# Optimization experiments

Hardware: AMD Instinct MI355X
Metric: run time of the kernel (lower is better)

## Reference

```python
import jax, jax.numpy as jnp
import numpy as np
import math

B, D, NSTEPS = 16384, 256, 5
TEMP, ALPHA, ALPHA_A, ETA, EPS = 2.0, 0.2, 0.5, 1.0e4, 1e-10


def setup_inputs() -> dict:
    key = jax.random.key(0)
    ks = jax.random.split(key, 7)
    x = jax.random.bernoulli(ks[0], 0.5, (B, D)).astype(jnp.float32)  # binary state
    x_a = jax.random.normal(ks[1], (B, D), jnp.float32)  # auxiliary (continuous)
    A = jax.random.normal(ks[2], (D, D), jnp.float32)
    W = 0.1 * (A + A.T) / math.sqrt(D)  # symmetric coupling of quadratic EBM
    b = 0.1 * jax.random.normal(ks[3], (D,), jnp.float32)
    rr = jax.random.uniform(ks[4], (NSTEPS, B, D), jnp.float32)  # flip uniforms
    noise = jax.random.normal(ks[5], (NSTEPS, B, D), jnp.float32)  # Langevin noise
    accept_u = jax.random.uniform(ks[6], (NSTEPS, B), jnp.float32)  # MH uniforms
    return {"x": x, "x_a": x_a, "W": W, "b": b, "rr": rr, "noise": noise, "accept_u": accept_u}


def reference(x, x_a, W, b, rr, noise, accept_u):
    term2 = 1.0 / (2.0 * ALPHA)

    def energy(z):  # model(z): quadratic EBM, [B]
        return 0.5 * jnp.einsum('bd,de,be->b', z, W, z) + z @ b

    def diff_fn(z):  # approx_difference_function / temp: grad_E(z) * -(2z-1) / temp
        return (z @ W + b) * -(2.0 * z - 1.0) / TEMP

    def agrad(z, za):  # auxillary_gradient_function(eta, z, za)
        return (z - za) / ETA

    def step(carry, inp):
        x_cur, x_a_cur = carry
        rr_i, noise_i, u_i = inp
        ga = agrad(x_cur, x_a_cur)
        gm = diff_fn(x_cur) - ga / TEMP * -(2.0 * x_cur - 1.0)
        # exp(t)/(exp(t)+1) == sigmoid(t)
        flip_prob = jax.nn.sigmoid(gm - term2)
        ind = (rr_i < flip_prob).astype(x_cur.dtype)
        x_delta = (1.0 - x_cur) * ind + x_cur * (1.0 - ind)
        x_delta_a = x_a_cur + 0.5 * ALPHA_A * ga + math.sqrt(ALPHA_A) * noise_i
        lp_forward = jnp.sum(jnp.log(flip_prob * ind + (1.0 - flip_prob) * (1.0 - ind) + EPS), axis=-1)
        ga2 = agrad(x_delta, x_delta_a)
        gm2 = diff_fn(x_delta) - ga2 / TEMP * -(2.0 * x_delta - 1.0)
        fp2 = jax.nn.sigmoid(gm2 - term2)
        lp_reverse = jnp.sum(jnp.log(fp2 * ind + (1.0 - fp2) * (1.0 - ind) + EPS), axis=-1)
        m_term = (energy(x_delta) - jnp.sum((x_delta - x_delta_a) ** 2, axis=1) / (2.0 * ETA)) \
               - (energy(x_cur) - jnp.sum((x_cur - x_a_cur) ** 2, axis=1) / (2.0 * ETA))
        add_rev = jnp.sum((x_a_cur - (x_delta_a + 0.5 * ALPHA_A * ga2)) ** 2, axis=1) / (-2.0 * ALPHA_A)
        add_fwd = jnp.sum((x_delta_a - (x_a_cur + 0.5 * ALPHA_A * ga)) ** 2, axis=1) / (-2.0 * ALPHA_A)
        la = m_term + add_rev - add_fwd + lp_reverse - lp_forward
        # exp(la) > u  <=>  la > log(u); avoids overflow of exp
        a = (la > jnp.log(u_i)).astype(x_cur.dtype)
        x_new = x_delta * a[:, None] + x_cur * (1.0 - a[:, None])
        xa_new = x_delta_a * a[:, None] + x_a_cur * (1.0 - a[:, None])
        return (x_new, xa_new), None

    (x_out, xa_out), _ = jax.lax.scan(step, (x, x_a), (rr, noise, accept_u))
    return x_out, xa_out
```

## Files before the change

### kernel.cpp

```cpp
#include <hip/hip_runtime.h>
#include <math.h>


namespace {

constexpr int kB = 16384;
constexpr int kD = 256;
constexpr int kSteps = 5;

typedef float v2f __attribute__((ext_vector_type(2)));
typedef float v4f __attribute__((ext_vector_type(4)));

__device__ __forceinline__ v4f nt_load4(const float* p) {
  return __builtin_nontemporal_load(reinterpret_cast<const v4f*>(p));
}
__device__ __forceinline__ void nt_store4(float* p, v4f v) {
  __builtin_nontemporal_store(v, reinterpret_cast<v4f*>(p));
}

__device__ __forceinline__ float wave_sum(float v) {
#pragma unroll
  for (int off = 32; off > 0; off >>= 1) v += __shfl_xor(v, off, 64);
  return v;
}

__device__ __forceinline__ float sigmoid_f(float t) {
  if (t >= 0.0f) {
    float e = expf(-t);
    return 1.0f / (1.0f + e);
  } else {
    float e = expf(t);
    return e / (1.0f + e);
  }
}

__global__ __launch_bounds__(256) void els_fused(
    const float* __restrict__ x_in, const float* __restrict__ xa_in,
    const float* __restrict__ W, const float* __restrict__ bvec,
    const float* __restrict__ rr, const float* __restrict__ noise,
    const float* __restrict__ accept_u, float* __restrict__ out) {
  const int lane = threadIdx.x & 63;
  const int row = blockIdx.x * 4 + (threadIdx.x >> 6);
  const int c0 = lane << 2;

  const v4f x4 = nt_load4(x_in + (size_t)row * kD + c0);
  const v4f a4 = nt_load4(xa_in + (size_t)row * kD + c0);
  const float4 b4 = *reinterpret_cast<const float4*>(bvec + c0);
  float xv[4] = {x4.x, x4.y, x4.z, x4.w};
  float xa[4] = {a4.x, a4.y, a4.z, a4.w};
  const float bv[4] = {b4.x, b4.y, b4.z, b4.w};
  v2f y01 = {0.0f, 0.0f}, y23 = {0.0f, 0.0f};

  v4f r4 = nt_load4(rr + (size_t)row * kD + c0);
  v4f n4 = nt_load4(noise + (size_t)row * kD + c0);
  float u = accept_u[row];

#pragma unroll
  for (int i = 0; i < 4; ++i) {
    unsigned long long m = __ballot(xv[i] > 0.5f);
    const int cnt = __popcll(m);
    int t = 0;
    for (; t + 8 <= cnt; t += 8) {
      int j[8];
#pragma unroll
      for (int q = 0; q < 8; ++q) { j[q] = __builtin_ctzll(m); m &= m - 1; }
      float4 w[8];
#pragma unroll
      for (int q = 0; q < 8; ++q)
        w[q] = *reinterpret_cast<const float4*>(W + (size_t)(4 * j[q] + i) * kD + c0);
#pragma unroll
      for (int q = 0; q < 8; ++q) {
        y01 += (v2f){w[q].x, w[q].y};
        y23 += (v2f){w[q].z, w[q].w};
      }
    }
    for (; t < cnt; ++t) {
      const int jj = __builtin_ctzll(m); m &= m - 1;
      const float4 w = *reinterpret_cast<const float4*>(W + (size_t)(4 * jj + i) * kD + c0);
      y01 += (v2f){w.x, w.y};
      y23 += (v2f){w.z, w.w};
    }
  }

  for (int step = 0; step < kSteps; ++step) {
    const float rrv[4] = {r4.x, r4.y, r4.z, r4.w};
    const float nzv[4] = {n4.x, n4.y, n4.z, n4.w};
    const float ucur = u;

    const int sn = (step + 1 < kSteps) ? step + 1 : step;
    const size_t offn = ((size_t)sn * kB + row) * kD + c0;
    r4 = nt_load4(rr + offn);
    n4 = nt_load4(noise + offn);
    u = accept_u[(size_t)sn * kB + row];

    const float yv[4] = {y01.x, y01.y, y23.x, y23.y};
    float ga[4], xd[4], xda[4];
    bool ind[4];
    float s_lpf = 0.f, s_xy = 0.f, s_xb = 0.f, s_sqc = 0.f, s_fwd = 0.f;
    unsigned long long fm[4], sm[4];

#pragma unroll
    for (int i = 0; i < 4; ++i) {
      ga[i] = (xv[i] - xa[i]) / 1.0e4f;
      const float sgn = 1.0f - 2.0f * xv[i];
      const float gm = (yv[i] + bv[i] - ga[i]) * sgn / 2.0f;
      const float p = sigmoid_f(gm - 2.5f);
      ind[i] = rrv[i] < p;
      xd[i] = ind[i] ? 1.0f - xv[i] : xv[i];
      xda[i] = xa[i] + 0.25f * ga[i] + 0.70710678118654752f * nzv[i];
      const float pr = ind[i] ? p : 1.0f - p;
      s_lpf += logf(pr + 1e-10f);
      s_xy += xv[i] * yv[i];
      s_xb += xv[i] * bv[i];
      const float dc = xv[i] - xa[i];
      s_sqc += dc * dc;
      const float fw = xda[i] - (xa[i] + 0.25f * ga[i]);
      s_fwd += fw * fw;
      fm[i] = __ballot(ind[i]);
      sm[i] = __ballot(xv[i] > 0.5f);
    }

    v2f y2lo = y01, y2hi = y23;
#pragma unroll
    for (int i = 0; i < 4; ++i) {
      unsigned long long m = fm[i];
      const int cnt = __popcll(m);
      int t = 0;
      for (; t + 4 <= cnt; t += 4) {
        int j[4];
#pragma unroll
        for (int q = 0; q < 4; ++q) { j[q] = __builtin_ctzll(m); m &= m - 1; }
        float4 w[4];
        float s[4];
#pragma unroll
        for (int q = 0; q < 4; ++q) {
          s[q] = ((sm[i] >> j[q]) & 1ull) ? -1.0f : 1.0f;
          w[q] = *reinterpret_cast<const float4*>(W + (size_t)(4 * j[q] + i) * kD + c0);
        }
#pragma unroll
        for (int q = 0; q < 4; ++q) {
          const v2f sv = {s[q], s[q]};
          y2lo = __builtin_elementwise_fma(sv, (v2f){w[q].x, w[q].y}, y2lo);
          y2hi = __builtin_elementwise_fma(sv, (v2f){w[q].z, w[q].w}, y2hi);
        }
      }
      for (; t < cnt; ++t) {
        const int jj = __builtin_ctzll(m); m &= m - 1;
        const float s = ((sm[i] >> jj) & 1ull) ? -1.0f : 1.0f;
        const float4 w = *reinterpret_cast<const float4*>(W + (size_t)(4 * jj + i) * kD + c0);
        const v2f sv = {s, s};
        y2lo = __builtin_elementwise_fma(sv, (v2f){w.x, w.y}, y2lo);
        y2hi = __builtin_elementwise_fma(sv, (v2f){w.z, w.w}, y2hi);
      }
    }

    const float y2v[4] = {y2lo.x, y2lo.y, y2hi.x, y2hi.y};
    float s_lpr = 0.f, s_xdy = 0.f, s_xdb = 0.f, s_sqn = 0.f, s_rev = 0.f;
#pragma unroll
    for (int i = 0; i < 4; ++i) {
      const float ga2 = (xd[i] - xda[i]) / 1.0e4f;
      const float sgn2 = 1.0f - 2.0f * xd[i];
      const float gm2 = (y2v[i] + bv[i] - ga2) * sgn2 / 2.0f;
      const float p2 = sigmoid_f(gm2 - 2.5f);
      const float pr2 = ind[i] ? p2 : 1.0f - p2;
      s_lpr += logf(pr2 + 1e-10f);
      s_xdy += xd[i] * y2v[i];
      s_xdb += xd[i] * bv[i];
      const float dn = xd[i] - xda[i];
      s_sqn += dn * dn;
      const float rv = xa[i] - (xda[i] + 0.25f * ga2);
      s_rev += rv * rv;
    }

    s_lpf = wave_sum(s_lpf);
    s_lpr = wave_sum(s_lpr);
    s_xy = wave_sum(s_xy);
    s_xb = wave_sum(s_xb);
    s_xdy = wave_sum(s_xdy);
    s_xdb = wave_sum(s_xdb);
    s_sqc = wave_sum(s_sqc);
    s_sqn = wave_sum(s_sqn);
    s_rev = wave_sum(s_rev);
    s_fwd = wave_sum(s_fwd);

    const float E_cur = 0.5f * s_xy + s_xb;
    const float E_new = 0.5f * s_xdy + s_xdb;
    const float m_term = (E_new - s_sqn / 2.0e4f) - (E_cur - s_sqc / 2.0e4f);
    const float la = m_term - s_rev + s_fwd + s_lpr - s_lpf;
    const bool acc = la > logf(ucur);

#pragma unroll
    for (int i = 0; i < 4; ++i) {
      xv[i] = acc ? xd[i] : xv[i];
      xa[i] = acc ? xda[i] : xa[i];
    }
    y01 = acc ? y2lo : y01;
    y23 = acc ? y2hi : y23;
  }

  const v4f ox = {xv[0], xv[1], xv[2], xv[3]};
  const v4f oa = {xa[0], xa[1], xa[2], xa[3]};
  nt_store4(out + (size_t)row * kD + c0, ox);
  nt_store4(out + (size_t)kB * kD + (size_t)row * kD + c0, oa);
}

}

extern "C" void kernel_launch(void* const* d_in, const int* in_sizes, int n_in,
                              void* d_out, int out_size, void* d_ws, size_t ws_size,
                              hipStream_t stream) {
  const float* x = (const float*)d_in[0];
  const float* xa = (const float*)d_in[1];
  const float* W = (const float*)d_in[2];
  const float* b = (const float*)d_in[3];
  const float* rr = (const float*)d_in[4];
  const float* noise = (const float*)d_in[5];
  const float* au = (const float*)d_in[6];
  float* out = (float*)d_out;

  dim3 grid(kB / 4);
  dim3 block(256);
  hipLaunchKernelGGL(els_fused, grid, block, 0, stream, x, xa, W, b, rr, noise,
                     au, out);
}
```

Before: 380.4 us.

## Stage half of W in LDS with 1024-thread blocks and prefetch global rows

Grows blocks to 16 waves and copies the first 128 rows of W (128 KB) into shared memory once per block. W-row gathers for the low half of each column mask are served from LDS, and the high half still comes from global/L2. A few global W rows are issued early so their latency overlaps with the LDS-side accumulation and the logf work. The large LDS footprint limits occupancy to about one block per CU, and each block pays a 128 KB fill before it can compute.

```diff
diff --git a/kernel.cpp b/kernel.cpp
--- a/kernel.cpp
+++ b/kernel.cpp
@@ -7,6 +7,8 @@
 constexpr int kB = 16384;
 constexpr int kD = 256;
 constexpr int kSteps = 5;
+constexpr int kLdsRows = 128;
+constexpr int kWaves = 16;
 
 typedef float v2f __attribute__((ext_vector_type(2)));
 typedef float v4f __attribute__((ext_vector_type(4)));
@@ -34,36 +36,95 @@
   }
 }
 
-__global__ __launch_bounds__(256) void els_fused(
+__global__ __launch_bounds__(1024) void els_fused(
     const float* __restrict__ x_in, const float* __restrict__ xa_in,
     const float* __restrict__ W, const float* __restrict__ bvec,
     const float* __restrict__ rr, const float* __restrict__ noise,
     const float* __restrict__ accept_u, float* __restrict__ out) {
-  const int lane = threadIdx.x & 63;
-  const int row = blockIdx.x * 4 + (threadIdx.x >> 6);
+  __shared__ float wlds[kLdsRows * kD];
+
+  const int tid = threadIdx.x;
+  const int lane = tid & 63;
+  const int row = blockIdx.x * kWaves + (tid >> 6);
   const int c0 = lane << 2;
 
   const v4f x4 = nt_load4(x_in + (size_t)row * kD + c0);
   const v4f a4 = nt_load4(xa_in + (size_t)row * kD + c0);
   const float4 b4 = *reinterpret_cast<const float4*>(bvec + c0);
+  v4f r4 = nt_load4(rr + (size_t)row * kD + c0);
+  v4f n4 = nt_load4(noise + (size_t)row * kD + c0);
+  float u = accept_u[row];
+
+  {
+    const float4* __restrict__ wsrc = reinterpret_cast<const float4*>(W);
+    float4* wdst = reinterpret_cast<float4*>(wlds);
+#pragma unroll
+    for (int k = 0; k < (kLdsRows * kD / 4) / 1024; ++k)
+      wdst[k * 1024 + tid] = wsrc[k * 1024 + tid];
+  }
+  __syncthreads();
+
   float xv[4] = {x4.x, x4.y, x4.z, x4.w};
   float xa[4] = {a4.x, a4.y, a4.z, a4.w};
   const float bv[4] = {b4.x, b4.y, b4.z, b4.w};
   v2f y01 = {0.0f, 0.0f}, y23 = {0.0f, 0.0f};
 
-  v4f r4 = nt_load4(rr + (size_t)row * kD + c0);
-  v4f n4 = nt_load4(noise + (size_t)row * kD + c0);
-  float u = accept_u[row];
-
 #pragma unroll
   for (int i = 0; i < 4; ++i) {
-    unsigned long long m = __ballot(xv[i] > 0.5f);
-    const int cnt = __popcll(m);
+    const unsigned long long m = __ballot(xv[i] > 0.5f);
+    const unsigned long long mlo = m & 0xffffffffull;
+    unsigned long long mh = m & 0xffffffff00000000ull;
+    const int hcnt = __popcll(mh);
+
+    float4 hwp[8];
+    const bool pre8 = hcnt >= 8;
+    if (pre8) {
+#pragma unroll
+      for (int q = 0; q < 8; ++q) {
+        const int j = __builtin_ctzll(mh); mh &= mh - 1;
+        hwp[q] = *reinterpret_cast<const float4*>(W + (size_t)(4 * j + i) * kD + c0);
+      }
+    }
+
+    {
+      unsigned long long ml = mlo;
+      const int cnt = __popcll(mlo);
+      int t = 0;
+      for (; t + 8 <= cnt; t += 8) {
+        int j[8];
+#pragma unroll
+        for (int q = 0; q < 8; ++q) { j[q] = __builtin_ctzll(ml); ml &= ml - 1; }
+        float4 w[8];
+#pragma unroll
+        for (int q = 0; q < 8; ++q)
+          w[q] = *reinterpret_cast<const float4*>(&wlds[(4 * j[q] + i) * kD + c0]);
+#pragma unroll
+        for (int q = 0; q < 8; ++q) {
+          y01 += (v2f){w[q].x, w[q].y};
+          y23 += (v2f){w[q].z, w[q].w};
+        }
+      }
+      for (; t < cnt; ++t) {
+        const int jj = __builtin_ctzll(ml); ml &= ml - 1;
+        const float4 w = *reinterpret_cast<const float4*>(&wlds[(4 * jj + i) * kD + c0]);
+        y01 += (v2f){w.x, w.y};
+        y23 += (v2f){w.z, w.w};
+      }
+    }
+
     int t = 0;
-    for (; t + 8 <= cnt; t += 8) {
+    if (pre8) {
+#pragma unroll
+      for (int q = 0; q < 8; ++q) {
+        y01 += (v2f){hwp[q].x, hwp[q].y};
+        y23 += (v2f){hwp[q].z, hwp[q].w};
+      }
+      t = 8;
+    }
+    for (; t + 8 <= hcnt; t += 8) {
       int j[8];
 #pragma unroll
-      for (int q = 0; q < 8; ++q) { j[q] = __builtin_ctzll(m); m &= m - 1; }
+      for (int q = 0; q < 8; ++q) { j[q] = __builtin_ctzll(mh); mh &= mh - 1; }
       float4 w[8];
 #pragma unroll
       for (int q = 0; q < 8; ++q)
@@ -74,8 +135,8 @@
         y23 += (v2f){w[q].z, w[q].w};
       }
     }
-    for (; t < cnt; ++t) {
-      const int jj = __builtin_ctzll(m); m &= m - 1;
+    for (; t < hcnt; ++t) {
+      const int jj = __builtin_ctzll(mh); mh &= mh - 1;
       const float4 w = *reinterpret_cast<const float4*>(W + (size_t)(4 * jj + i) * kD + c0);
       y01 += (v2f){w.x, w.y};
       y23 += (v2f){w.z, w.w};
@@ -94,9 +155,8 @@
     u = accept_u[(size_t)sn * kB + row];
 
     const float yv[4] = {y01.x, y01.y, y23.x, y23.y};
-    float ga[4], xd[4], xda[4];
+    float ga[4], xd[4], xda[4], pr[4];
     bool ind[4];
-    float s_lpf = 0.f, s_xy = 0.f, s_xb = 0.f, s_sqc = 0.f, s_fwd = 0.f;
     unsigned long long fm[4], sm[4];
 
 #pragma unroll
@@ -108,49 +168,117 @@
       ind[i] = rrv[i] < p;
       xd[i] = ind[i] ? 1.0f - xv[i] : xv[i];
       xda[i] = xa[i] + 0.25f * ga[i] + 0.70710678118654752f * nzv[i];
-      const float pr = ind[i] ? p : 1.0f - p;
-      s_lpf += logf(pr + 1e-10f);
+      pr[i] = ind[i] ? p : 1.0f - p;
+      fm[i] = __ballot(ind[i]);
+      sm[i] = __ballot(xv[i] > 0.5f);
+    }
+
+    unsigned long long mh_rem[4];
+    int hcnt[4], hpre[4];
+    float4 hw[4][2];
+    float hs[4][2];
+#pragma unroll
+    for (int i = 0; i < 4; ++i) {
+      unsigned long long mh = fm[i] & 0xffffffff00000000ull;
+      hcnt[i] = __popcll(mh);
+      const int np = hcnt[i] < 2 ? hcnt[i] : 2;
+#pragma unroll
+      for (int q = 0; q < 2; ++q) {
+        if (q < np) {
+          const int j = __builtin_ctzll(mh); mh &= mh - 1;
+          hs[i][q] = ((sm[i] >> j) & 1ull) ? -1.0f : 1.0f;
+          hw[i][q] = *reinterpret_cast<const float4*>(W + (size_t)(4 * j + i) * kD + c0);
+        }
+      }
+      mh_rem[i] = mh;
+      hpre[i] = np;
+    }
+
+    float s_lpf = 0.f, s_xy = 0.f, s_xb = 0.f, s_sqc = 0.f, s_fwd = 0.f;
+#pragma unroll
+    for (int i = 0; i < 4; ++i) {
+      s_lpf += logf(pr[i] + 1e-10f);
       s_xy += xv[i] * yv[i];
       s_xb += xv[i] * bv[i];
       const float dc = xv[i] - xa[i];
       s_sqc += dc * dc;
       const float fw = xda[i] - (xa[i] + 0.25f * ga[i]);
       s_fwd += fw * fw;
-      fm[i] = __ballot(ind[i]);
-      sm[i] = __ballot(xv[i] > 0.5f);
     }
 
     v2f y2lo = y01, y2hi = y23;
 #pragma unroll
     for (int i = 0; i < 4; ++i) {
-      unsigned long long m = fm[i];
-      const int cnt = __popcll(m);
-      int t = 0;
-      for (; t + 4 <= cnt; t += 4) {
-        int j[4];
-#pragma unroll
-        for (int q = 0; q < 4; ++q) { j[q] = __builtin_ctzll(m); m &= m - 1; }
-        float4 w[4];
-        float s[4];
-#pragma unroll
-        for (int q = 0; q < 4; ++q) {
-          s[q] = ((sm[i] >> j[q]) & 1ull) ? -1.0f : 1.0f;
-          w[q] = *reinterpret_cast<const float4*>(W + (size_t)(4 * j[q] + i) * kD + c0);
-        }
-#pragma unroll
-        for (int q = 0; q < 4; ++q) {
-          const v2f sv = {s[q], s[q]};
-          y2lo = __builtin_elementwise_fma(sv, (v2f){w[q].x, w[q].y}, y2lo);
-          y2hi = __builtin_elementwise_fma(sv, (v2f){w[q].z, w[q].w}, y2hi);
-        }
-      }
-      for (; t < cnt; ++t) {
-        const int jj = __builtin_ctzll(m); m &= m - 1;
-        const float s = ((sm[i] >> jj) & 1ull) ? -1.0f : 1.0f;
-        const float4 w = *reinterpret_cast<const float4*>(W + (size_t)(4 * jj + i) * kD + c0);
-        const v2f sv = {s, s};
-        y2lo = __builtin_elementwise_fma(sv, (v2f){w.x, w.y}, y2lo);
-        y2hi = __builtin_elementwise_fma(sv, (v2f){w.z, w.w}, y2hi);
+      {
+        unsigned long long ml = fm[i] & 0xffffffffull;
+        const int cnt = __popcll(ml);
+        int t = 0;
+        for (; t + 4 <= cnt; t += 4) {
+          int j[4];
+#pragma unroll
+          for (int q = 0; q < 4; ++q) { j[q] = __builtin_ctzll(ml); ml &= ml - 1; }
+          float4 w[4];
+          float s[4];
+#pragma unroll
+          for (int q = 0; q < 4; ++q) {
+            s[q] = ((sm[i] >> j[q]) & 1ull) ? -1.0f : 1.0f;
+            w[q] = *reinterpret_cast<const float4*>(&wlds[(4 * j[q] + i) * kD + c0]);
+          }
+#pragma unroll
+          for (int q = 0; q < 4; ++q) {
+            const v2f sv = {s[q], s[q]};
+            y2lo = __builtin_elementwise_fma(sv, (v2f){w[q].x, w[q].y}, y2lo);
+            y2hi = __builtin_elementwise_fma(sv, (v2f){w[q].z, w[q].w}, y2hi);
+          }
+        }
+        for (; t < cnt; ++t) {
+          const int jj = __builtin_ctzll(ml); ml &= ml - 1;
+          const float s = ((sm[i] >> jj) & 1ull) ? -1.0f : 1.0f;
+          const float4 w = *reinterpret_cast<const float4*>(&wlds[(4 * jj + i) * kD + c0]);
+          const v2f sv = {s, s};
+          y2lo = __builtin_elementwise_fma(sv, (v2f){w.x, w.y}, y2lo);
+          y2hi = __builtin_elementwise_fma(sv, (v2f){w.z, w.w}, y2hi);
+        }
+      }
+
+#pragma unroll
+      for (int q = 0; q < 2; ++q) {
+        if (q < hpre[i]) {
+          const v2f sv = {hs[i][q], hs[i][q]};
+          y2lo = __builtin_elementwise_fma(sv, (v2f){hw[i][q].x, hw[i][q].y}, y2lo);
+          y2hi = __builtin_elementwise_fma(sv, (v2f){hw[i][q].z, hw[i][q].w}, y2hi);
+        }
+      }
+      {
+        unsigned long long mh = mh_rem[i];
+        const int hc = hcnt[i];
+        int t = hpre[i];
+        for (; t + 4 <= hc; t += 4) {
+          int j[4];
+#pragma unroll
+          for (int q = 0; q < 4; ++q) { j[q] = __builtin_ctzll(mh); mh &= mh - 1; }
+          float4 w[4];
+          float s[4];
+#pragma unroll
+          for (int q = 0; q < 4; ++q) {
+            s[q] = ((sm[i] >> j[q]) & 1ull) ? -1.0f : 1.0f;
+            w[q] = *reinterpret_cast<const float4*>(W + (size_t)(4 * j[q] + i) * kD + c0);
+          }
+#pragma unroll
+          for (int q = 0; q < 4; ++q) {
+            const v2f sv = {s[q], s[q]};
+            y2lo = __builtin_elementwise_fma(sv, (v2f){w[q].x, w[q].y}, y2lo);
+            y2hi = __builtin_elementwise_fma(sv, (v2f){w[q].z, w[q].w}, y2hi);
+          }
+        }
+        for (; t < hc; ++t) {
+          const int jj = __builtin_ctzll(mh); mh &= mh - 1;
+          const float s = ((sm[i] >> jj) & 1ull) ? -1.0f : 1.0f;
+          const float4 w = *reinterpret_cast<const float4*>(W + (size_t)(4 * jj + i) * kD + c0);
+          const v2f sv = {s, s};
+          y2lo = __builtin_elementwise_fma(sv, (v2f){w.x, w.y}, y2lo);
+          y2hi = __builtin_elementwise_fma(sv, (v2f){w.z, w.w}, y2hi);
+        }
       }
     }
 
@@ -218,8 +346,8 @@
   const float* au = (const float*)d_in[6];
   float* out = (float*)d_out;
 
-  dim3 grid(kB / 4);
-  dim3 block(256);
+  dim3 grid(kB / kWaves);
+  dim3 block(1024);
   hipLaunchKernelGGL(els_fused, grid, block, 0, stream, x, xa, W, b, rr, noise,
                      au, out);
 }
```

Result: slower. 390.4 us (+2.6%).

## Double-buffer sparse W row gathers to overlap loads with accumulation

Applied to the files above, without the earlier changes.

Replaces the batched gather loops over set bits with ping-pong register buffers of eight W rows, so the next batch of loads is issued before the current batch is accumulated. This applies both to the initial x@W pass and to the per-step flip-delta update. In the step loop it also moves the forward-sum computation between the first prefetches and their consumption to hide load latency. Holding two buffers of eight float4 values raises register pressure and may lower occupancy, and the predicated fetch/consume code adds some branching.

```diff
diff --git a/kernel.cpp b/kernel.cpp
--- a/kernel.cpp
+++ b/kernel.cpp
@@ -42,6 +42,7 @@
   const int lane = threadIdx.x & 63;
   const int row = blockIdx.x * 4 + (threadIdx.x >> 6);
   const int c0 = lane << 2;
+  const float* __restrict__ Wc = W + c0;
 
   const v4f x4 = nt_load4(x_in + (size_t)row * kD + c0);
   const v4f a4 = nt_load4(xa_in + (size_t)row * kD + c0);
@@ -58,27 +59,36 @@
 #pragma unroll
   for (int i = 0; i < 4; ++i) {
     unsigned long long m = __ballot(xv[i] > 0.5f);
-    const int cnt = __popcll(m);
-    int t = 0;
-    for (; t + 8 <= cnt; t += 8) {
-      int j[8];
-#pragma unroll
-      for (int q = 0; q < 8; ++q) { j[q] = __builtin_ctzll(m); m &= m - 1; }
-      float4 w[8];
+    float4 bufA[8], bufB[8];
+    int na = 0, nb = 0;
+    auto fetch8 = [&](float4 (&buf)[8]) -> int {
+      int n = 0;
+#pragma unroll
+      for (int q = 0; q < 8; ++q) {
+        if (m) {
+          const int j = __builtin_ctzll(m); m &= m - 1;
+          buf[q] = *reinterpret_cast<const float4*>(Wc + (size_t)(4 * j + i) * kD);
+          ++n;
+        }
+      }
+      return n;
+    };
+    auto cons8 = [&](const float4 (&buf)[8], int n) {
 #pragma unroll
       for (int q = 0; q < 8; ++q)
-        w[q] = *reinterpret_cast<const float4*>(W + (size_t)(4 * j[q] + i) * kD + c0);
-#pragma unroll
-      for (int q = 0; q < 8; ++q) {
-        y01 += (v2f){w[q].x, w[q].y};
-        y23 += (v2f){w[q].z, w[q].w};
-      }
-    }
-    for (; t < cnt; ++t) {
-      const int jj = __builtin_ctzll(m); m &= m - 1;
-      const float4 w = *reinterpret_cast<const float4*>(W + (size_t)(4 * jj + i) * kD + c0);
-      y01 += (v2f){w.x, w.y};
-      y23 += (v2f){w.z, w.w};
+        if (q < n) {
+          y01 += (v2f){buf[q].x, buf[q].y};
+          y23 += (v2f){buf[q].z, buf[q].w};
+        }
+    };
+    na = fetch8(bufA);
+    for (;;) {
+      if (!m) { cons8(bufA, na); break; }
+      nb = fetch8(bufB);
+      cons8(bufA, na);
+      if (!m) { cons8(bufB, nb); break; }
+      na = fetch8(bufA);
+      cons8(bufB, nb);
     }
   }
 
@@ -94,9 +104,8 @@
     u = accept_u[(size_t)sn * kB + row];
 
     const float yv[4] = {y01.x, y01.y, y23.x, y23.y};
-    float ga[4], xd[4], xda[4];
+    float ga[4], xd[4], xda[4], pr[4];
     bool ind[4];
-    float s_lpf = 0.f, s_xy = 0.f, s_xb = 0.f, s_sqc = 0.f, s_fwd = 0.f;
     unsigned long long fm[4], sm[4];
 
 #pragma unroll
@@ -108,51 +117,73 @@
       ind[i] = rrv[i] < p;
       xd[i] = ind[i] ? 1.0f - xv[i] : xv[i];
       xda[i] = xa[i] + 0.25f * ga[i] + 0.70710678118654752f * nzv[i];
-      const float pr = ind[i] ? p : 1.0f - p;
-      s_lpf += logf(pr + 1e-10f);
+      pr[i] = ind[i] ? p : 1.0f - p;
+      fm[i] = __ballot(ind[i]);
+      sm[i] = __ballot(xv[i] > 0.5f);
+    }
+
+    float4 wP[8], wQ[8];
+    int jP[8], jQ[8];
+    int nP = 0, nQ = 0;
+    unsigned long long mP = 0, mQ = 0;
+    auto gfetch = [&](int i, float4 (&wb)[8], int (&jb)[8], int& n,
+                      unsigned long long& mr) {
+      unsigned long long mm = fm[i];
+      n = 0;
+#pragma unroll
+      for (int q = 0; q < 8; ++q) {
+        if (mm) {
+          const int j = __builtin_ctzll(mm); mm &= mm - 1;
+          jb[q] = j;
+          wb[q] = *reinterpret_cast<const float4*>(Wc + (size_t)(4 * j + i) * kD);
+          ++n;
+        }
+      }
+      mr = mm;
+    };
+
+    v2f y2lo = y01, y2hi = y23;
+    auto gcons = [&](int i, const float4 (&wb)[8], const int (&jb)[8], int n,
+                     unsigned long long mr) {
+#pragma unroll
+      for (int q = 0; q < 8; ++q)
+        if (q < n) {
+          const float s = ((sm[i] >> jb[q]) & 1ull) ? -1.0f : 1.0f;
+          const v2f sv = {s, s};
+          y2lo = __builtin_elementwise_fma(sv, (v2f){wb[q].x, wb[q].y}, y2lo);
+          y2hi = __builtin_elementwise_fma(sv, (v2f){wb[q].z, wb[q].w}, y2hi);
+        }
+      while (mr) {
+        const int j = __builtin_ctzll(mr); mr &= mr - 1;
+        const float s = ((sm[i] >> j) & 1ull) ? -1.0f : 1.0f;
+        const float4 w = *reinterpret_cast<const float4*>(Wc + (size_t)(4 * j + i) * kD);
+        const v2f sv = {s, s};
+        y2lo = __builtin_elementwise_fma(sv, (v2f){w.x, w.y}, y2lo);
+        y2hi = __builtin_elementwise_fma(sv, (v2f){w.z, w.w}, y2hi);
+      }
+    };
+
+    gfetch(0, wP, jP, nP, mP);
+    gfetch(1, wQ, jQ, nQ, mQ);
+
+    float s_lpf = 0.f, s_xy = 0.f, s_xb = 0.f, s_sqc = 0.f, s_fwd = 0.f;
+#pragma unroll
+    for (int i = 0; i < 4; ++i) {
+      s_lpf += logf(pr[i] + 1e-10f);
       s_xy += xv[i] * yv[i];
       s_xb += xv[i] * bv[i];
       const float dc = xv[i] - xa[i];
       s_sqc += dc * dc;
       const float fw = xda[i] - (xa[i] + 0.25f * ga[i]);
       s_fwd += fw * fw;
-      fm[i] = __ballot(ind[i]);
-      sm[i] = __ballot(xv[i] > 0.5f);
-    }
-
-    v2f y2lo = y01, y2hi = y23;
-#pragma unroll
-    for (int i = 0; i < 4; ++i) {
-      unsigned long long m = fm[i];
-      const int cnt = __popcll(m);
-      int t = 0;
-      for (; t + 4 <= cnt; t += 4) {
-        int j[4];
-#pragma unroll
-        for (int q = 0; q < 4; ++q) { j[q] = __builtin_ctzll(m); m &= m - 1; }
-        float4 w[4];
-        float s[4];
-#pragma unroll
-        for (int q = 0; q < 4; ++q) {
-          s[q] = ((sm[i] >> j[q]) & 1ull) ? -1.0f : 1.0f;
-          w[q] = *reinterpret_cast<const float4*>(W + (size_t)(4 * j[q] + i) * kD + c0);
-        }
-#pragma unroll
-        for (int q = 0; q < 4; ++q) {
-          const v2f sv = {s[q], s[q]};
-          y2lo = __builtin_elementwise_fma(sv, (v2f){w[q].x, w[q].y}, y2lo);
-          y2hi = __builtin_elementwise_fma(sv, (v2f){w[q].z, w[q].w}, y2hi);
-        }
-      }
-      for (; t < cnt; ++t) {
-        const int jj = __builtin_ctzll(m); m &= m - 1;
-        const float s = ((sm[i] >> jj) & 1ull) ? -1.0f : 1.0f;
-        const float4 w = *reinterpret_cast<const float4*>(W + (size_t)(4 * jj + i) * kD + c0);
-        const v2f sv = {s, s};
-        y2lo = __builtin_elementwise_fma(sv, (v2f){w.x, w.y}, y2lo);
-        y2hi = __builtin_elementwise_fma(sv, (v2f){w.z, w.w}, y2hi);
-      }
-    }
+    }
+
+    gcons(0, wP, jP, nP, mP);
+    gfetch(2, wP, jP, nP, mP);
+    gcons(1, wQ, jQ, nQ, mQ);
+    gfetch(3, wQ, jQ, nQ, mQ);
+    gcons(2, wP, jP, nP, mP);
+    gcons(3, wQ, jQ, nQ, mQ);
 
     const float y2v[4] = {y2lo.x, y2lo.y, y2hi.x, y2hi.y};
     float s_lpr = 0.f, s_xdy = 0.f, s_xdb = 0.f, s_sqn = 0.f, s_rev = 0.f;
```

Result: slower. 406.3 us (+6.8%).

## Stream W rows through LDS ring with async global_load_lds double buffering

Applied to the files above, without the earlier changes.

Replaces the direct per-lane global loads of selected W rows with asynchronous global-to-LDS DMA into a per-wave double-buffered ring, with explicit vmcnt waits so the next chunk's loads overlap the current chunk's accumulation. The four per-column sparse loops are merged into one stream over all selected rows. The prefetch of the next step's rr/noise/u moves after the sparse gather so it does not compete with the vmcnt accounting. This adds 32KB of LDS per block, which can lower occupancy, and relies on manual waitcnt correctness.

```diff
diff --git a/kernel.cpp b/kernel.cpp
--- a/kernel.cpp
+++ b/kernel.cpp
@@ -10,6 +10,7 @@
 
 typedef float v2f __attribute__((ext_vector_type(2)));
 typedef float v4f __attribute__((ext_vector_type(4)));
+typedef unsigned long long u64;
 
 __device__ __forceinline__ v4f nt_load4(const float* p) {
   return __builtin_nontemporal_load(reinterpret_cast<const v4f*>(p));
@@ -34,14 +35,46 @@
   }
 }
 
+__device__ __forceinline__ void dma16(const float* g, float* l) {
+  __builtin_amdgcn_global_load_lds(
+      (const __attribute__((address_space(1))) void*)g,
+      (__attribute__((address_space(3))) void*)l, 16, 0, 0);
+}
+
+__device__ __forceinline__ int snext(u64& m0, u64& m1, u64& m2, u64& m3) {
+  if (m0) { const int j = __builtin_ctzll(m0); m0 &= m0 - 1; return 4 * j + 0; }
+  if (m1) { const int j = __builtin_ctzll(m1); m1 &= m1 - 1; return 4 * j + 1; }
+  if (m2) { const int j = __builtin_ctzll(m2); m2 &= m2 - 1; return 4 * j + 2; }
+  { const int j = __builtin_ctzll(m3); m3 &= m3 - 1; return 4 * j + 3; }
+}
+
+__device__ __forceinline__ float snext_sign(u64& m0, u64& m1, u64& m2, u64& m3,
+                                            u64 s0, u64 s1, u64 s2, u64 s3) {
+  if (m0) { const int j = __builtin_ctzll(m0); m0 &= m0 - 1;
+            return ((s0 >> j) & 1ull) ? -1.0f : 1.0f; }
+  if (m1) { const int j = __builtin_ctzll(m1); m1 &= m1 - 1;
+            return ((s1 >> j) & 1ull) ? -1.0f : 1.0f; }
+  if (m2) { const int j = __builtin_ctzll(m2); m2 &= m2 - 1;
+            return ((s2 >> j) & 1ull) ? -1.0f : 1.0f; }
+  { const int j = __builtin_ctzll(m3); m3 &= m3 - 1;
+    return ((s3 >> j) & 1ull) ? -1.0f : 1.0f; }
+}
+
 __global__ __launch_bounds__(256) void els_fused(
     const float* __restrict__ x_in, const float* __restrict__ xa_in,
     const float* __restrict__ W, const float* __restrict__ bvec,
     const float* __restrict__ rr, const float* __restrict__ noise,
     const float* __restrict__ accept_u, float* __restrict__ out) {
-  const int lane = threadIdx.x & 63;
-  const int row = blockIdx.x * 4 + (threadIdx.x >> 6);
+  __shared__ float ring[4][8 * kD];
+
+  const int tid = threadIdx.x;
+  const int lane = tid & 63;
+  const int wid = tid >> 6;
+  const int row = blockIdx.x * 4 + wid;
   const int c0 = lane << 2;
+  float* const ringw = &ring[wid][0];
+  const float* const ringl = ringw + c0;
+  const float* const Wl = W + c0;
 
   const v4f x4 = nt_load4(x_in + (size_t)row * kD + c0);
   const v4f a4 = nt_load4(xa_in + (size_t)row * kD + c0);
@@ -55,30 +88,46 @@
   v4f n4 = nt_load4(noise + (size_t)row * kD + c0);
   float u = accept_u[row];
 
-#pragma unroll
-  for (int i = 0; i < 4; ++i) {
-    unsigned long long m = __ballot(xv[i] > 0.5f);
-    const int cnt = __popcll(m);
-    int t = 0;
-    for (; t + 8 <= cnt; t += 8) {
-      int j[8];
-#pragma unroll
-      for (int q = 0; q < 8; ++q) { j[q] = __builtin_ctzll(m); m &= m - 1; }
-      float4 w[8];
-#pragma unroll
-      for (int q = 0; q < 8; ++q)
-        w[q] = *reinterpret_cast<const float4*>(W + (size_t)(4 * j[q] + i) * kD + c0);
-#pragma unroll
-      for (int q = 0; q < 8; ++q) {
-        y01 += (v2f){w[q].x, w[q].y};
-        y23 += (v2f){w[q].z, w[q].w};
+  {
+    u64 b0 = __ballot(xv[0] > 0.5f);
+    u64 b1 = __ballot(xv[1] > 0.5f);
+    u64 b2 = __ballot(xv[2] > 0.5f);
+    u64 b3 = __ballot(xv[3] > 0.5f);
+    const int total = __popcll(b0) + __popcll(b1) + __popcll(b2) + __popcll(b3);
+    const int chunks = (total + 3) >> 2;
+    u64 a0 = b0, a1 = b1, a2 = b2, a3 = b3;
+    int issued = 0;
+    auto issue4 = [&](int bank) {
+#pragma unroll
+      for (int q = 0; q < 4; ++q) {
+        int d = 0;
+        if (issued < total) { d = snext(a0, a1, a2, a3); ++issued; }
+        dma16(Wl + (size_t)d * kD, ringw + (bank * 4 + q) * kD);
       }
-    }
-    for (; t < cnt; ++t) {
-      const int jj = __builtin_ctzll(m); m &= m - 1;
-      const float4 w = *reinterpret_cast<const float4*>(W + (size_t)(4 * jj + i) * kD + c0);
-      y01 += (v2f){w.x, w.y};
-      y23 += (v2f){w.z, w.w};
+    };
+    if (total > 0) {
+      issue4(0);
+      int bk = 0, consumed = 0;
+      for (int k = 0; k < chunks; ++k) {
+        if (k + 1 < chunks) {
+          issue4(bk ^ 1);
+          asm volatile("s_waitcnt vmcnt(4)" ::: "memory");
+        } else {
+          asm volatile("s_waitcnt vmcnt(0)" ::: "memory");
+        }
+        __builtin_amdgcn_sched_barrier(0);
+        const int n = (total - consumed < 4) ? (total - consumed) : 4;
+#pragma unroll
+        for (int q = 0; q < 4; ++q) {
+          if (q < n) {
+            const v4f w = *reinterpret_cast<const v4f*>(ringl + (bk * 4 + q) * kD);
+            y01 += (v2f){w.x, w.y};
+            y23 += (v2f){w.z, w.w};
+          }
+        }
+        consumed += n;
+        bk ^= 1;
+      }
     }
   }
 
@@ -87,17 +136,11 @@
     const float nzv[4] = {n4.x, n4.y, n4.z, n4.w};
     const float ucur = u;
 
-    const int sn = (step + 1 < kSteps) ? step + 1 : step;
-    const size_t offn = ((size_t)sn * kB + row) * kD + c0;
-    r4 = nt_load4(rr + offn);
-    n4 = nt_load4(noise + offn);
-    u = accept_u[(size_t)sn * kB + row];
-
     const float yv[4] = {y01.x, y01.y, y23.x, y23.y};
     float ga[4], xd[4], xda[4];
     bool ind[4];
     float s_lpf = 0.f, s_xy = 0.f, s_xb = 0.f, s_sqc = 0.f, s_fwd = 0.f;
-    unsigned long long fm[4], sm[4];
+    u64 fm0, fm1, fm2, fm3, sm0, sm1, sm2, sm3;
 
 #pragma unroll
     for (int i = 0; i < 4; ++i) {
@@ -116,43 +159,64 @@
       s_sqc += dc * dc;
       const float fw = xda[i] - (xa[i] + 0.25f * ga[i]);
       s_fwd += fw * fw;
-      fm[i] = __ballot(ind[i]);
-      sm[i] = __ballot(xv[i] > 0.5f);
+      const u64 fmb = __ballot(ind[i]);
+      const u64 smb = __ballot(xv[i] > 0.5f);
+      if (i == 0) { fm0 = fmb; sm0 = smb; }
+      else if (i == 1) { fm1 = fmb; sm1 = smb; }
+      else if (i == 2) { fm2 = fmb; sm2 = smb; }
+      else { fm3 = fmb; sm3 = smb; }
     }
 
     v2f y2lo = y01, y2hi = y23;
-#pragma unroll
-    for (int i = 0; i < 4; ++i) {
-      unsigned long long m = fm[i];
-      const int cnt = __popcll(m);
-      int t = 0;
-      for (; t + 4 <= cnt; t += 4) {
-        int j[4];
-#pragma unroll
-        for (int q = 0; q < 4; ++q) { j[q] = __builtin_ctzll(m); m &= m - 1; }
-        float4 w[4];
-        float s[4];
+    {
+      const int total = __popcll(fm0) + __popcll(fm1) + __popcll(fm2) + __popcll(fm3);
+      const int chunks = (total + 3) >> 2;
+      u64 a0 = fm0, a1 = fm1, a2 = fm2, a3 = fm3;
+      u64 c0m = fm0, c1m = fm1, c2m = fm2, c3m = fm3;
+      int issued = 0;
+      auto issue4 = [&](int bank) {
 #pragma unroll
         for (int q = 0; q < 4; ++q) {
-          s[q] = ((sm[i] >> j[q]) & 1ull) ? -1.0f : 1.0f;
-          w[q] = *reinterpret_cast<const float4*>(W + (size_t)(4 * j[q] + i) * kD + c0);
-        }
-#pragma unroll
-        for (int q = 0; q < 4; ++q) {
-          const v2f sv = {s[q], s[q]};
-          y2lo = __builtin_elementwise_fma(sv, (v2f){w[q].x, w[q].y}, y2lo);
-          y2hi = __builtin_elementwise_fma(sv, (v2f){w[q].z, w[q].w}, y2hi);
+          int d = 0;
+          if (issued < total) { d = snext(a0, a1, a2, a3); ++issued; }
+          dma16(Wl + (size_t)d * kD, ringw + (bank * 4 + q) * kD);
+        }
+      };
+      if (total > 0) {
+        issue4(0);
+        int bk = 0, consumed = 0;
+        for (int k = 0; k < chunks; ++k) {
+          if (k + 1 < chunks) {
+            issue4(bk ^ 1);
+            asm volatile("s_waitcnt vmcnt(4)" ::: "memory");
+          } else {
+            asm volatile("s_waitcnt vmcnt(0)" ::: "memory");
+          }
+          __builtin_amdgcn_sched_barrier(0);
+          const int n = (total - consumed < 4) ? (total - consumed) : 4;
+#pragma unroll
+          for (int q = 0; q < 4; ++q) {
+            if (q < n) {
+              const float s =
+                  snext_sign(c0m, c1m, c2m, c3m, sm0, sm1, sm2, sm3);
+              const v4f w =
+                  *reinterpret_cast<const v4f*>(ringl + (bk * 4 + q) * kD);
+              const v2f sv = {s, s};
+              y2lo = __builtin_elementwise_fma(sv, (v2f){w.x, w.y}, y2lo);
+              y2hi = __builtin_elementwise_fma(sv, (v2f){w.z, w.w}, y2hi);
+            }
+          }
+          consumed += n;
+          bk ^= 1;
         }
       }
-      for (; t < cnt; ++t) {
-        const int jj = __builtin_ctzll(m); m &= m - 1;
-        const float s = ((sm[i] >> jj) & 1ull) ? -1.0f : 1.0f;
-        const float4 w = *reinterpret_cast<const float4*>(W + (size_t)(4 * jj + i) * kD + c0);
-        const v2f sv = {s, s};
-        y2lo = __builtin_elementwise_fma(sv, (v2f){w.x, w.y}, y2lo);
-        y2hi = __builtin_elementwise_fma(sv, (v2f){w.z, w.w}, y2hi);
-      }
-    }
+    }
+
+    const int sn = (step + 1 < kSteps) ? step + 1 : step;
+    const size_t offn = ((size_t)sn * kB + row) * kD + c0;
+    r4 = nt_load4(rr + offn);
+    n4 = nt_load4(noise + offn);
+    u = accept_u[(size_t)sn * kB + row];
 
     const float y2v[4] = {y2lo.x, y2lo.y, y2hi.x, y2hi.y};
     float s_lpr = 0.f, s_xdy = 0.f, s_xdb = 0.f, s_sqn = 0.f, s_rev = 0.f;
```

After: 705.7 us. 1.86x slower.
